# Kernel tuning notes

Measured on AMD Instinct MI355X. Metric: run time of the kernel, lower is better.

The kernel has to match this reference:

```python
import jax, jax.numpy as jnp
import numpy as np
import itertools


def setup_inputs() -> dict:
    key = jax.random.key(0)
    k1, k2 = jax.random.split(key)
    # Learned 3D LUT: [3, D, D, D], values in [0,1] like an identity/learned color LUT
    lut = jax.random.uniform(k1, (3, 33, 33, 33), dtype=jnp.float32)
    # Input RGB image batch in [0,1): [B, 3, H, W]
    x = jax.random.uniform(k2, (4, 3, 1080, 1920), dtype=jnp.float32)
    return {"lut": lut, "x": x}


def reference(lut, x):
    # Faithful JAX version of the trilinear.forward CUDA kernel:
    # per-pixel 8-corner trilinear interpolation into a [3, D, D, D] LUT.
    dim = lut.shape[-1]
    binsize = 1.000001 / (dim - 1)

    r, g, b = x[:, 0], x[:, 1], x[:, 2]  # each [B, H, W]

    inv = 1.0 / binsize
    rid = jnp.floor(r * inv).astype(jnp.int32)
    gid = jnp.floor(g * inv).astype(jnp.int32)
    bid = jnp.floor(b * inv).astype(jnp.int32)
    # fractional offsets within the cell
    fr = r * inv - rid
    fg = g * inv - gid
    fb = b * inv - bid
    # clamp so id+1 stays in range (kernel assumes x in [0,1))
    rid = jnp.clip(rid, 0, dim - 2)
    gid = jnp.clip(gid, 0, dim - 2)
    bid = jnp.clip(bid, 0, dim - 2)

    # LUT layout matches flattened index id_r + id_g*dim + id_b*dim^2
    # i.e. lut[c, b_idx, g_idx, r_idx].
    out = jnp.zeros((3,) + r.shape, dtype=x.dtype)  # [3, B, H, W]
    for db, dg, dr in itertools.product((0, 1), repeat=3):
        wr = fr if dr else (1.0 - fr)
        wg = fg if dg else (1.0 - fg)
        wb = fb if db else (1.0 - fb)
        w = wr * wg * wb  # [B, H, W]
        corner = lut[:, bid + db, gid + dg, rid + dr]  # [3, B, H, W] gather
        out = out + w[None] * corner

    return jnp.transpose(out, (1, 0, 2, 3))  # [B, 3, H, W]
```

## Files before the change

kernel.cpp:

```cpp
#include <hip/hip_runtime.h>
#include <hip/hip_fp16.h>

#define P_PLANE (1080*1920)
#define LUT_C   35937
#define N_IMG   4
#define SMEM_WORDS 35937
#define SMEM_BYTES (SMEM_WORDS * 4)

typedef float fvec4 __attribute__((ext_vector_type(4)));

__global__ __launch_bounds__(256) void build_lin_u8(const float* __restrict__ lut,
                                                    unsigned int* __restrict__ T) {
    int i = blockIdx.x * blockDim.x + threadIdx.x;
    if (i >= LUT_C) return;
    unsigned int r = (unsigned int)__float2int_rn(lut[i] * 255.0f);
    unsigned int g = (unsigned int)__float2int_rn(lut[LUT_C + i] * 255.0f);
    unsigned int b = (unsigned int)__float2int_rn(lut[2 * LUT_C + i] * 255.0f);
    T[i] = r | (g << 8) | (b << 16);
}

__device__ __forceinline__ float ub0(unsigned int e) { return (float)(e & 255u); }
__device__ __forceinline__ float ub1(unsigned int e) { return (float)((e >> 8) & 255u); }
__device__ __forceinline__ float ub2(unsigned int e) { return (float)((e >> 16) & 255u); }

__global__ __launch_bounds__(1024) void apply_lut_lds(const float* __restrict__ x,
                                                      const unsigned int* __restrict__ T,
                                                      float* __restrict__ out) {
    extern __shared__ unsigned int s_lut[];
    const int tid = threadIdx.x;

    {
        const uint4* Tv = (const uint4*)T;
        uint4* sv = (uint4*)s_lut;
        for (int i = tid; i < SMEM_WORDS / 4; i += blockDim.x) sv[i] = Tv[i];
        if (tid == 0) s_lut[SMEM_WORDS - 1] = T[SMEM_WORDS - 1];
    }
    __syncthreads();

    const float inv = (float)(1.0 / (1.000001 / 32.0));
    const float qs = 1.0f / 255.0f;
    const int QPI = P_PLANE / 4;
    const int total = N_IMG * QPI;

    for (int q = blockIdx.x * blockDim.x + tid; q < total; q += gridDim.x * blockDim.x) {
        int n  = q / QPI;
        int p4 = q - n * QPI;
        size_t base = (size_t)n * 3 * P_PLANE + (size_t)p4 * 4;

        fvec4 r4 = *(const fvec4*)(x + base);
        fvec4 g4 = *(const fvec4*)(x + base + P_PLANE);
        fvec4 b4 = *(const fvec4*)(x + base + 2 * P_PLANE);

        fvec4 vR, vG, vB;

#pragma unroll
        for (int i = 0; i < 4; ++i) {
            float tr = r4[i] * inv;
            float tg = g4[i] * inv;
            float tb = b4[i] * inv;
            float fr_ = floorf(tr), fg_ = floorf(tg), fb_ = floorf(tb);
            float fr = tr - fr_, fg = tg - fg_, fb = tb - fb_;
            int ri = min(max((int)fr_, 0), 31);
            int gi = min(max((int)fg_, 0), 31);
            int bi = min(max((int)fb_, 0), 31);
            int idx = bi * 1089 + gi * 33 + ri;

            unsigned int e000 = s_lut[idx],        e001 = s_lut[idx + 1];
            unsigned int e010 = s_lut[idx + 33],   e011 = s_lut[idx + 34];
            unsigned int e100 = s_lut[idx + 1089], e101 = s_lut[idx + 1090];
            unsigned int e110 = s_lut[idx + 1122], e111 = s_lut[idx + 1123];

            float wr1 = fr, wr0 = 1.0f - fr;
            float wg1 = fg, wg0 = 1.0f - fg;
            float wb1 = fb * qs, wb0 = (1.0f - fb) * qs;
            float w00 = wb0 * wg0, w01 = wb0 * wg1, w10 = wb1 * wg0, w11 = wb1 * wg1;
            float w000 = w00 * wr0, w001 = w00 * wr1;
            float w010 = w01 * wr0, w011 = w01 * wr1;
            float w100 = w10 * wr0, w101 = w10 * wr1;
            float w110 = w11 * wr0, w111 = w11 * wr1;

            float aR, aG, aB;
            aR = w000 * ub0(e000);            aG = w000 * ub1(e000);            aB = w000 * ub2(e000);
            aR = fmaf(w001, ub0(e001), aR);   aG = fmaf(w001, ub1(e001), aG);   aB = fmaf(w001, ub2(e001), aB);
            aR = fmaf(w010, ub0(e010), aR);   aG = fmaf(w010, ub1(e010), aG);   aB = fmaf(w010, ub2(e010), aB);
            aR = fmaf(w011, ub0(e011), aR);   aG = fmaf(w011, ub1(e011), aG);   aB = fmaf(w011, ub2(e011), aB);
            aR = fmaf(w100, ub0(e100), aR);   aG = fmaf(w100, ub1(e100), aG);   aB = fmaf(w100, ub2(e100), aB);
            aR = fmaf(w101, ub0(e101), aR);   aG = fmaf(w101, ub1(e101), aG);   aB = fmaf(w101, ub2(e101), aB);
            aR = fmaf(w110, ub0(e110), aR);   aG = fmaf(w110, ub1(e110), aG);   aB = fmaf(w110, ub2(e110), aB);
            aR = fmaf(w111, ub0(e111), aR);   aG = fmaf(w111, ub1(e111), aG);   aB = fmaf(w111, ub2(e111), aB);

            vR[i] = aR; vG[i] = aG; vB[i] = aB;
        }

        __builtin_nontemporal_store(vR, (fvec4*)(out + base));
        __builtin_nontemporal_store(vG, (fvec4*)(out + base + P_PLANE));
        __builtin_nontemporal_store(vB, (fvec4*)(out + base + 2 * P_PLANE));
    }
}

__global__ __launch_bounds__(256) void build_table(const float* __restrict__ lut,
                                                   uint4* __restrict__ T) {
    int cell = blockIdx.x * blockDim.x + threadIdx.x;
    int rid = cell & 31;
    int gid = (cell >> 5) & 31;
    int bid = cell >> 10;
    const float* b0 = lut + bid * 1089 + gid * 33 + rid;
    uint4 q[4];
    __half* h = (__half*)q;
#pragma unroll
    for (int k = 0; k < 8; ++k) {
        int off = (k >> 2) * 1089 + ((k >> 1) & 1) * 33 + (k & 1);
        h[k * 4 + 0] = __float2half(b0[off]);
        h[k * 4 + 1] = __float2half(b0[LUT_C + off]);
        h[k * 4 + 2] = __float2half(b0[2 * LUT_C + off]);
        h[k * 4 + 3] = __float2half(0.0f);
    }
    uint4* dst = T + (size_t)cell * 4;
    dst[0] = q[0]; dst[1] = q[1]; dst[2] = q[2]; dst[3] = q[3];
}

__device__ __forceinline__ void acc_chunk(const uint4& q, float wA, float wB,
                                          float& aR, float& aG, float& aB) {
    const __half* h = (const __half*)&q;
    aR = fmaf(wA, __half2float(h[0]), fmaf(wB, __half2float(h[4]), aR));
    aG = fmaf(wA, __half2float(h[1]), fmaf(wB, __half2float(h[5]), aG));
    aB = fmaf(wA, __half2float(h[2]), fmaf(wB, __half2float(h[6]), aB));
}

__global__ __launch_bounds__(256) void apply_lut(const float* __restrict__ x,
                                                 const __half* __restrict__ T,
                                                 float* __restrict__ out) {
    const float inv = (float)(1.0 / (1.000001 / 32.0));
    int n  = blockIdx.y;
    int i4 = blockIdx.x * blockDim.x + threadIdx.x;
    size_t base = (size_t)n * 3 * P_PLANE + (size_t)i4 * 4;

    float4 r4 = *(const float4*)(x + base);
    float4 g4 = *(const float4*)(x + base + P_PLANE);
    float4 b4 = *(const float4*)(x + base + 2 * P_PLANE);

    float r[4] = {r4.x, r4.y, r4.z, r4.w};
    float g[4] = {g4.x, g4.y, g4.z, g4.w};
    float b[4] = {b4.x, b4.y, b4.z, b4.w};
    float oR[4], oG[4], oB[4];

#pragma unroll
    for (int i = 0; i < 4; ++i) {
        float tr = r[i] * inv;
        float tg = g[i] * inv;
        float tb = b[i] * inv;
        float fr_ = floorf(tr), fg_ = floorf(tg), fb_ = floorf(tb);
        float fr = tr - fr_, fg = tg - fg_, fb = tb - fb_;
        int ri = min(max((int)fr_, 0), 31);
        int gi = min(max((int)fg_, 0), 31);
        int bi = min(max((int)fb_, 0), 31);

        const uint4* cp = (const uint4*)(T + ((size_t)(((bi << 5) | gi) << 5 | ri) << 5));
        uint4 q0 = cp[0], q1 = cp[1], q2 = cp[2], q3 = cp[3];

        float wr1 = fr, wr0 = 1.0f - fr;
        float wg1 = fg, wg0 = 1.0f - fg;
        float wb1 = fb, wb0 = 1.0f - fb;
        float w00 = wb0 * wg0, w01 = wb0 * wg1, w10 = wb1 * wg0, w11 = wb1 * wg1;

        float aR = 0.f, aG = 0.f, aB = 0.f;
        acc_chunk(q0, w00 * wr0, w00 * wr1, aR, aG, aB);
        acc_chunk(q1, w01 * wr0, w01 * wr1, aR, aG, aB);
        acc_chunk(q2, w10 * wr0, w10 * wr1, aR, aG, aB);
        acc_chunk(q3, w11 * wr0, w11 * wr1, aR, aG, aB);

        oR[i] = aR; oG[i] = aG; oB[i] = aB;
    }

    *(float4*)(out + base)               = make_float4(oR[0], oR[1], oR[2], oR[3]);
    *(float4*)(out + base + P_PLANE)     = make_float4(oG[0], oG[1], oG[2], oG[3]);
    *(float4*)(out + base + 2 * P_PLANE) = make_float4(oB[0], oB[1], oB[2], oB[3]);
}

extern "C" void kernel_launch(void* const* d_in, const int* in_sizes, int n_in,
                              void* d_out, int out_size, void* d_ws, size_t ws_size,
                              hipStream_t stream) {
    const float* lut = (const float*)d_in[0];
    const float* x   = (const float*)d_in[1];
    float* out = (float*)d_out;

    int dev = 0;
    (void)hipGetDevice(&dev);
    int max_shm = 0;
    (void)hipDeviceGetAttribute(&max_shm, hipDeviceAttributeMaxSharedMemoryPerBlock, dev);
    static_assert(SMEM_BYTES == 143748, "lut lds size");
    (void)hipFuncSetAttribute((const void*)apply_lut_lds,
                              hipFuncAttributeMaxDynamicSharedMemorySize, SMEM_BYTES);

    const size_t lin_bytes = (size_t)SMEM_BYTES;
    if (max_shm >= SMEM_BYTES && ws_size >= lin_bytes) {
        unsigned int* T = (unsigned int*)d_ws;
        build_lin_u8<<<(LUT_C + 255) / 256, 256, 0, stream>>>(lut, T);
        apply_lut_lds<<<256, 1024, SMEM_BYTES, stream>>>(x, T, out);
    } else {
        const size_t table_bytes = (size_t)32768 * 64;
        __half* T = (__half*)d_ws;
        build_table<<<128, 256, 0, stream>>>(lut, (uint4*)T);
        apply_lut<<<dim3(P_PLANE / (4 * 256), N_IMG), 256, 0, stream>>>(x, T, out);
    }
}
```

Baseline: 187.3 us.

## Software-pipeline input loads and process eight pixels per thread in LDS LUT kernel

The grid-stride loop is restructured so each thread handles eight pixels per iteration and prefetches the next iteration's input vectors before the current iteration's LDS gathers and FMAs run. All 64 LDS reads are issued before any arithmetic, which gives more memory-level parallelism. The host-side attribute queries are cached in a static variable, and launch_bounds gains a minimum-blocks hint. The cost is much higher register pressure, which could cause spills or reduce occupancy.

```diff
diff --git a/kernel.cpp b/kernel.cpp
--- a/kernel.cpp
+++ b/kernel.cpp
@@ -6,6 +6,9 @@
 #define N_IMG   4
 #define SMEM_WORDS 35937
 #define SMEM_BYTES (SMEM_WORDS * 4)
+
+#define PPI         (P_PLANE / 8)
+#define TOTAL_PAIRS (N_IMG * PPI)
 
 typedef float fvec4 __attribute__((ext_vector_type(4)));
 
@@ -23,9 +26,9 @@
 __device__ __forceinline__ float ub1(unsigned int e) { return (float)((e >> 8) & 255u); }
 __device__ __forceinline__ float ub2(unsigned int e) { return (float)((e >> 16) & 255u); }
 
-__global__ __launch_bounds__(1024) void apply_lut_lds(const float* __restrict__ x,
-                                                      const unsigned int* __restrict__ T,
-                                                      float* __restrict__ out) {
+__global__ __launch_bounds__(1024, 4) void apply_lut_lds(const float* __restrict__ x,
+                                                         const unsigned int* __restrict__ T,
+                                                         float* __restrict__ out) {
     extern __shared__ unsigned int s_lut[];
     const int tid = threadIdx.x;
 
@@ -39,62 +42,102 @@
 
     const float inv = (float)(1.0 / (1.000001 / 32.0));
     const float qs = 1.0f / 255.0f;
-    const int QPI = P_PLANE / 4;
-    const int total = N_IMG * QPI;
-
-    for (int q = blockIdx.x * blockDim.x + tid; q < total; q += gridDim.x * blockDim.x) {
-        int n  = q / QPI;
-        int p4 = q - n * QPI;
-        size_t base = (size_t)n * 3 * P_PLANE + (size_t)p4 * 4;
-
-        fvec4 r4 = *(const fvec4*)(x + base);
-        fvec4 g4 = *(const fvec4*)(x + base + P_PLANE);
-        fvec4 b4 = *(const fvec4*)(x + base + 2 * P_PLANE);
-
-        fvec4 vR, vG, vB;
-
-#pragma unroll
-        for (int i = 0; i < 4; ++i) {
-            float tr = r4[i] * inv;
-            float tg = g4[i] * inv;
-            float tb = b4[i] * inv;
+    const int stride = gridDim.x * blockDim.x;
+
+    int p = blockIdx.x * blockDim.x + tid;
+    if (p >= TOTAL_PAIRS) return;
+
+    size_t base;
+    {
+        int n = p / PPI;
+        base = (size_t)n * (3 * P_PLANE) + (size_t)(p - n * PPI) * 8;
+    }
+    fvec4 rA = *(const fvec4*)(x + base);
+    fvec4 rB = *(const fvec4*)(x + base + 4);
+    fvec4 gA = *(const fvec4*)(x + base + P_PLANE);
+    fvec4 gB = *(const fvec4*)(x + base + P_PLANE + 4);
+    fvec4 bA = *(const fvec4*)(x + base + 2 * P_PLANE);
+    fvec4 bB = *(const fvec4*)(x + base + 2 * P_PLANE + 4);
+
+    while (true) {
+        int pn = p + stride;
+        int pc = (pn < TOTAL_PAIRS) ? pn : p;
+        size_t nbase;
+        {
+            int n = pc / PPI;
+            nbase = (size_t)n * (3 * P_PLANE) + (size_t)(pc - n * PPI) * 8;
+        }
+        fvec4 nrA = *(const fvec4*)(x + nbase);
+        fvec4 nrB = *(const fvec4*)(x + nbase + 4);
+        fvec4 ngA = *(const fvec4*)(x + nbase + P_PLANE);
+        fvec4 ngB = *(const fvec4*)(x + nbase + P_PLANE + 4);
+        fvec4 nbA = *(const fvec4*)(x + nbase + 2 * P_PLANE);
+        fvec4 nbB = *(const fvec4*)(x + nbase + 2 * P_PLANE + 4);
+
+        int   idx[8];
+        float fr[8], fg[8], fb[8];
+#pragma unroll
+        for (int j = 0; j < 8; ++j) {
+            float r = (j < 4) ? rA[j] : rB[j - 4];
+            float g = (j < 4) ? gA[j] : gB[j - 4];
+            float b = (j < 4) ? bA[j] : bB[j - 4];
+            float tr = r * inv, tg = g * inv, tb = b * inv;
             float fr_ = floorf(tr), fg_ = floorf(tg), fb_ = floorf(tb);
-            float fr = tr - fr_, fg = tg - fg_, fb = tb - fb_;
+            fr[j] = tr - fr_; fg[j] = tg - fg_; fb[j] = tb - fb_;
             int ri = min(max((int)fr_, 0), 31);
             int gi = min(max((int)fg_, 0), 31);
             int bi = min(max((int)fb_, 0), 31);
-            int idx = bi * 1089 + gi * 33 + ri;
-
-            unsigned int e000 = s_lut[idx],        e001 = s_lut[idx + 1];
-            unsigned int e010 = s_lut[idx + 33],   e011 = s_lut[idx + 34];
-            unsigned int e100 = s_lut[idx + 1089], e101 = s_lut[idx + 1090];
-            unsigned int e110 = s_lut[idx + 1122], e111 = s_lut[idx + 1123];
-
-            float wr1 = fr, wr0 = 1.0f - fr;
-            float wg1 = fg, wg0 = 1.0f - fg;
-            float wb1 = fb * qs, wb0 = (1.0f - fb) * qs;
+            idx[j] = bi * 1089 + gi * 33 + ri;
+        }
+
+        unsigned int e[8][8];
+#pragma unroll
+        for (int j = 0; j < 8; ++j) {
+            int i0 = idx[j];
+            int i1 = idx[j] + 1089;
+            e[j][0] = s_lut[i0];       e[j][1] = s_lut[i0 + 1];
+            e[j][2] = s_lut[i0 + 33];  e[j][3] = s_lut[i0 + 34];
+            e[j][4] = s_lut[i1];       e[j][5] = s_lut[i1 + 1];
+            e[j][6] = s_lut[i1 + 33];  e[j][7] = s_lut[i1 + 34];
+        }
+
+        fvec4 oRA, oRB, oGA, oGB, oBA, oBB;
+#pragma unroll
+        for (int j = 0; j < 8; ++j) {
+            float wr1 = fr[j], wr0 = 1.0f - fr[j];
+            float wg1 = fg[j], wg0 = 1.0f - fg[j];
+            float wb1 = fb[j] * qs, wb0 = (1.0f - fb[j]) * qs;
             float w00 = wb0 * wg0, w01 = wb0 * wg1, w10 = wb1 * wg0, w11 = wb1 * wg1;
             float w000 = w00 * wr0, w001 = w00 * wr1;
             float w010 = w01 * wr0, w011 = w01 * wr1;
             float w100 = w10 * wr0, w101 = w10 * wr1;
             float w110 = w11 * wr0, w111 = w11 * wr1;
 
-            float aR, aG, aB;
-            aR = w000 * ub0(e000);            aG = w000 * ub1(e000);            aB = w000 * ub2(e000);
-            aR = fmaf(w001, ub0(e001), aR);   aG = fmaf(w001, ub1(e001), aG);   aB = fmaf(w001, ub2(e001), aB);
-            aR = fmaf(w010, ub0(e010), aR);   aG = fmaf(w010, ub1(e010), aG);   aB = fmaf(w010, ub2(e010), aB);
-            aR = fmaf(w011, ub0(e011), aR);   aG = fmaf(w011, ub1(e011), aG);   aB = fmaf(w011, ub2(e011), aB);
-            aR = fmaf(w100, ub0(e100), aR);   aG = fmaf(w100, ub1(e100), aG);   aB = fmaf(w100, ub2(e100), aB);
-            aR = fmaf(w101, ub0(e101), aR);   aG = fmaf(w101, ub1(e101), aG);   aB = fmaf(w101, ub2(e101), aB);
-            aR = fmaf(w110, ub0(e110), aR);   aG = fmaf(w110, ub1(e110), aG);   aB = fmaf(w110, ub2(e110), aB);
-            aR = fmaf(w111, ub0(e111), aR);   aG = fmaf(w111, ub1(e111), aG);   aB = fmaf(w111, ub2(e111), aB);
-
-            vR[i] = aR; vG[i] = aG; vB[i] = aB;
-        }
-
-        __builtin_nontemporal_store(vR, (fvec4*)(out + base));
-        __builtin_nontemporal_store(vG, (fvec4*)(out + base + P_PLANE));
-        __builtin_nontemporal_store(vB, (fvec4*)(out + base + 2 * P_PLANE));
+            float aR = w000 * ub0(e[j][0]);
+            float aG = w000 * ub1(e[j][0]);
+            float aB = w000 * ub2(e[j][0]);
+            aR = fmaf(w001, ub0(e[j][1]), aR); aG = fmaf(w001, ub1(e[j][1]), aG); aB = fmaf(w001, ub2(e[j][1]), aB);
+            aR = fmaf(w010, ub0(e[j][2]), aR); aG = fmaf(w010, ub1(e[j][2]), aG); aB = fmaf(w010, ub2(e[j][2]), aB);
+            aR = fmaf(w011, ub0(e[j][3]), aR); aG = fmaf(w011, ub1(e[j][3]), aG); aB = fmaf(w011, ub2(e[j][3]), aB);
+            aR = fmaf(w100, ub0(e[j][4]), aR); aG = fmaf(w100, ub1(e[j][4]), aG); aB = fmaf(w100, ub2(e[j][4]), aB);
+            aR = fmaf(w101, ub0(e[j][5]), aR); aG = fmaf(w101, ub1(e[j][5]), aG); aB = fmaf(w101, ub2(e[j][5]), aB);
+            aR = fmaf(w110, ub0(e[j][6]), aR); aG = fmaf(w110, ub1(e[j][6]), aG); aB = fmaf(w110, ub2(e[j][6]), aB);
+            aR = fmaf(w111, ub0(e[j][7]), aR); aG = fmaf(w111, ub1(e[j][7]), aG); aB = fmaf(w111, ub2(e[j][7]), aB);
+
+            if (j < 4) { oRA[j] = aR;     oGA[j] = aG;     oBA[j] = aB; }
+            else       { oRB[j - 4] = aR; oGB[j - 4] = aG; oBB[j - 4] = aB; }
+        }
+
+        __builtin_nontemporal_store(oRA, (fvec4*)(out + base));
+        __builtin_nontemporal_store(oRB, (fvec4*)(out + base + 4));
+        __builtin_nontemporal_store(oGA, (fvec4*)(out + base + P_PLANE));
+        __builtin_nontemporal_store(oGB, (fvec4*)(out + base + P_PLANE + 4));
+        __builtin_nontemporal_store(oBA, (fvec4*)(out + base + 2 * P_PLANE));
+        __builtin_nontemporal_store(oBB, (fvec4*)(out + base + 2 * P_PLANE + 4));
+
+        if (pn >= TOTAL_PAIRS) break;
+        p = pn; base = nbase;
+        rA = nrA; rB = nrB; gA = ngA; gB = ngB; bA = nbA; bB = nbB;
     }
 }
 
@@ -184,13 +227,16 @@
     const float* x   = (const float*)d_in[1];
     float* out = (float*)d_out;
 
-    int dev = 0;
-    (void)hipGetDevice(&dev);
-    int max_shm = 0;
-    (void)hipDeviceGetAttribute(&max_shm, hipDeviceAttributeMaxSharedMemoryPerBlock, dev);
-    static_assert(SMEM_BYTES == 143748, "lut lds size");
-    (void)hipFuncSetAttribute((const void*)apply_lut_lds,
-                              hipFuncAttributeMaxDynamicSharedMemorySize, SMEM_BYTES);
+    static int max_shm = -1;
+    if (max_shm < 0) {
+        int dev = 0;
+        (void)hipGetDevice(&dev);
+        (void)hipDeviceGetAttribute(&max_shm, hipDeviceAttributeMaxSharedMemoryPerBlock, dev);
+        static_assert(SMEM_BYTES == 143748, "lut lds size");
+        (void)hipFuncSetAttribute((const void*)apply_lut_lds,
+                                  hipFuncAttributeMaxDynamicSharedMemorySize, SMEM_BYTES);
+        if (max_shm < 0) max_shm = 0;
+    }
 
     const size_t lin_bytes = (size_t)SMEM_BYTES;
     if (max_shm >= SMEM_BYTES && ws_size >= lin_bytes) {
@@ -198,7 +244,6 @@
         build_lin_u8<<<(LUT_C + 255) / 256, 256, 0, stream>>>(lut, T);
         apply_lut_lds<<<256, 1024, SMEM_BYTES, stream>>>(x, T, out);
     } else {
-        const size_t table_bytes = (size_t)32768 * 64;
         __half* T = (__half*)d_ws;
         build_table<<<128, 256, 0, stream>>>(lut, (uint4*)T);
         apply_lut<<<dim3(P_PLANE / (4 * 256), N_IMG), 256, 0, stream>>>(x, T, out);
```

Result: slower. 205.8 us (+9.9%).

## Replace LDS-staged LUT with per-cell packed u8 corner table in global memory

Applied to the files above, without the earlier changes.

Builds a per-cell table holding all 8 corners as packed u8 RGB (32 bytes per cell) and gathers it with two 16-byte global loads per pixel, instead of staging the whole LUT into 140KB of LDS per block and doing 8 scattered LDS reads. This removes the per-block LDS fill and the occupancy limit of one large block per CU, relying on the 1MB table staying cache-resident. It also caches the device-attribute queries in a static and drops the old half-precision fallback path, so if the workspace is too small and LDS is insufficient nothing is launched.

```diff
diff --git a/kernel.cpp b/kernel.cpp
--- a/kernel.cpp
+++ b/kernel.cpp
@@ -7,45 +7,47 @@
 #define SMEM_WORDS 35937
 #define SMEM_BYTES (SMEM_WORDS * 4)
 
+#define N_CELLS   32768
+#define CELL_BYTES 32
+#define TABLE_BYTES ((size_t)N_CELLS * CELL_BYTES)
+
 typedef float fvec4 __attribute__((ext_vector_type(4)));
-
-__global__ __launch_bounds__(256) void build_lin_u8(const float* __restrict__ lut,
-                                                    unsigned int* __restrict__ T) {
-    int i = blockIdx.x * blockDim.x + threadIdx.x;
-    if (i >= LUT_C) return;
-    unsigned int r = (unsigned int)__float2int_rn(lut[i] * 255.0f);
-    unsigned int g = (unsigned int)__float2int_rn(lut[LUT_C + i] * 255.0f);
-    unsigned int b = (unsigned int)__float2int_rn(lut[2 * LUT_C + i] * 255.0f);
-    T[i] = r | (g << 8) | (b << 16);
-}
 
 __device__ __forceinline__ float ub0(unsigned int e) { return (float)(e & 255u); }
 __device__ __forceinline__ float ub1(unsigned int e) { return (float)((e >> 8) & 255u); }
 __device__ __forceinline__ float ub2(unsigned int e) { return (float)((e >> 16) & 255u); }
 
-__global__ __launch_bounds__(1024) void apply_lut_lds(const float* __restrict__ x,
-                                                      const unsigned int* __restrict__ T,
-                                                      float* __restrict__ out) {
-    extern __shared__ unsigned int s_lut[];
-    const int tid = threadIdx.x;
-
-    {
-        const uint4* Tv = (const uint4*)T;
-        uint4* sv = (uint4*)s_lut;
-        for (int i = tid; i < SMEM_WORDS / 4; i += blockDim.x) sv[i] = Tv[i];
-        if (tid == 0) s_lut[SMEM_WORDS - 1] = T[SMEM_WORDS - 1];
-    }
-    __syncthreads();
-
+__global__ __launch_bounds__(256) void build_cell_u8(const float* __restrict__ lut,
+                                                     uint4* __restrict__ T) {
+    int c = blockIdx.x * blockDim.x + threadIdx.x;
+    if (c >= N_CELLS) return;
+    int ri = c & 31, gi = (c >> 5) & 31, bi = c >> 10;
+    int idx = bi * 1089 + gi * 33 + ri;
+    unsigned int w[8];
+#pragma unroll
+    for (int k = 0; k < 8; ++k) {
+        int off = idx + (k & 1) + ((k >> 1) & 1) * 33 + ((k >> 2) & 1) * 1089;
+        unsigned int r = (unsigned int)__float2int_rn(lut[off] * 255.0f);
+        unsigned int g = (unsigned int)__float2int_rn(lut[LUT_C + off] * 255.0f);
+        unsigned int b = (unsigned int)__float2int_rn(lut[2 * LUT_C + off] * 255.0f);
+        w[k] = r | (g << 8) | (b << 16);
+    }
+    T[(size_t)c * 2]     = make_uint4(w[0], w[1], w[2], w[3]);
+    T[(size_t)c * 2 + 1] = make_uint4(w[4], w[5], w[6], w[7]);
+}
+
+__global__ __launch_bounds__(256, 8) void apply_lut_cell(const float* __restrict__ x,
+                                                         const uint4* __restrict__ T,
+                                                         float* __restrict__ out) {
     const float inv = (float)(1.0 / (1.000001 / 32.0));
     const float qs = 1.0f / 255.0f;
     const int QPI = P_PLANE / 4;
     const int total = N_IMG * QPI;
-
-    for (int q = blockIdx.x * blockDim.x + tid; q < total; q += gridDim.x * blockDim.x) {
-        int n  = q / QPI;
-        int p4 = q - n * QPI;
-        size_t base = (size_t)n * 3 * P_PLANE + (size_t)p4 * 4;
+    const int stride = gridDim.x * blockDim.x;
+
+    for (int q = blockIdx.x * blockDim.x + threadIdx.x; q < total; q += stride) {
+        int n = q / QPI;
+        size_t base = (size_t)n * (3 * P_PLANE) + (size_t)(q - n * QPI) * 4;
 
         fvec4 r4 = *(const fvec4*)(x + base);
         fvec4 g4 = *(const fvec4*)(x + base + P_PLANE);
@@ -63,12 +65,11 @@
             int ri = min(max((int)fr_, 0), 31);
             int gi = min(max((int)fg_, 0), 31);
             int bi = min(max((int)fb_, 0), 31);
-            int idx = bi * 1089 + gi * 33 + ri;
-
-            unsigned int e000 = s_lut[idx],        e001 = s_lut[idx + 1];
-            unsigned int e010 = s_lut[idx + 33],   e011 = s_lut[idx + 34];
-            unsigned int e100 = s_lut[idx + 1089], e101 = s_lut[idx + 1090];
-            unsigned int e110 = s_lut[idx + 1122], e111 = s_lut[idx + 1123];
+            int c = (bi << 10) | (gi << 5) | ri;
+
+            const uint4* cp = T + (size_t)c * 2;
+            uint4 lo = cp[0];
+            uint4 hi = cp[1];
 
             float wr1 = fr, wr0 = 1.0f - fr;
             float wg1 = fg, wg0 = 1.0f - fg;
@@ -79,15 +80,16 @@
             float w100 = w10 * wr0, w101 = w10 * wr1;
             float w110 = w11 * wr0, w111 = w11 * wr1;
 
-            float aR, aG, aB;
-            aR = w000 * ub0(e000);            aG = w000 * ub1(e000);            aB = w000 * ub2(e000);
-            aR = fmaf(w001, ub0(e001), aR);   aG = fmaf(w001, ub1(e001), aG);   aB = fmaf(w001, ub2(e001), aB);
-            aR = fmaf(w010, ub0(e010), aR);   aG = fmaf(w010, ub1(e010), aG);   aB = fmaf(w010, ub2(e010), aB);
-            aR = fmaf(w011, ub0(e011), aR);   aG = fmaf(w011, ub1(e011), aG);   aB = fmaf(w011, ub2(e011), aB);
-            aR = fmaf(w100, ub0(e100), aR);   aG = fmaf(w100, ub1(e100), aG);   aB = fmaf(w100, ub2(e100), aB);
-            aR = fmaf(w101, ub0(e101), aR);   aG = fmaf(w101, ub1(e101), aG);   aB = fmaf(w101, ub2(e101), aB);
-            aR = fmaf(w110, ub0(e110), aR);   aG = fmaf(w110, ub1(e110), aG);   aB = fmaf(w110, ub2(e110), aB);
-            aR = fmaf(w111, ub0(e111), aR);   aG = fmaf(w111, ub1(e111), aG);   aB = fmaf(w111, ub2(e111), aB);
+            float aR = w000 * ub0(lo.x);
+            float aG = w000 * ub1(lo.x);
+            float aB = w000 * ub2(lo.x);
+            aR = fmaf(w001, ub0(lo.y), aR); aG = fmaf(w001, ub1(lo.y), aG); aB = fmaf(w001, ub2(lo.y), aB);
+            aR = fmaf(w010, ub0(lo.z), aR); aG = fmaf(w010, ub1(lo.z), aG); aB = fmaf(w010, ub2(lo.z), aB);
+            aR = fmaf(w011, ub0(lo.w), aR); aG = fmaf(w011, ub1(lo.w), aG); aB = fmaf(w011, ub2(lo.w), aB);
+            aR = fmaf(w100, ub0(hi.x), aR); aG = fmaf(w100, ub1(hi.x), aG); aB = fmaf(w100, ub2(hi.x), aB);
+            aR = fmaf(w101, ub0(hi.y), aR); aG = fmaf(w101, ub1(hi.y), aG); aB = fmaf(w101, ub2(hi.y), aB);
+            aR = fmaf(w110, ub0(hi.z), aR); aG = fmaf(w110, ub1(hi.z), aG); aB = fmaf(w110, ub2(hi.z), aB);
+            aR = fmaf(w111, ub0(hi.w), aR); aG = fmaf(w111, ub1(hi.w), aG); aB = fmaf(w111, ub2(hi.w), aB);
 
             vR[i] = aR; vG[i] = aG; vB[i] = aB;
         }
@@ -98,83 +100,83 @@
     }
 }
 
-__global__ __launch_bounds__(256) void build_table(const float* __restrict__ lut,
-                                                   uint4* __restrict__ T) {
-    int cell = blockIdx.x * blockDim.x + threadIdx.x;
-    int rid = cell & 31;
-    int gid = (cell >> 5) & 31;
-    int bid = cell >> 10;
-    const float* b0 = lut + bid * 1089 + gid * 33 + rid;
-    uint4 q[4];
-    __half* h = (__half*)q;
+__global__ __launch_bounds__(256) void build_lin_u8(const float* __restrict__ lut,
+                                                    unsigned int* __restrict__ T) {
+    int i = blockIdx.x * blockDim.x + threadIdx.x;
+    if (i >= LUT_C) return;
+    unsigned int r = (unsigned int)__float2int_rn(lut[i] * 255.0f);
+    unsigned int g = (unsigned int)__float2int_rn(lut[LUT_C + i] * 255.0f);
+    unsigned int b = (unsigned int)__float2int_rn(lut[2 * LUT_C + i] * 255.0f);
+    T[i] = r | (g << 8) | (b << 16);
+}
+
+__global__ __launch_bounds__(1024, 4) void apply_lut_lds(const float* __restrict__ x,
+                                                         const unsigned int* __restrict__ T,
+                                                         float* __restrict__ out) {
+    extern __shared__ unsigned int s_lut[];
+    const int tid = threadIdx.x;
+    {
+        const uint4* Tv = (const uint4*)T;
+        uint4* sv = (uint4*)s_lut;
+        for (int i = tid; i < SMEM_WORDS / 4; i += blockDim.x) sv[i] = Tv[i];
+        if (tid == 0) s_lut[SMEM_WORDS - 1] = T[SMEM_WORDS - 1];
+    }
+    __syncthreads();
+
+    const float inv = (float)(1.0 / (1.000001 / 32.0));
+    const float qs = 1.0f / 255.0f;
+    const int QPI = P_PLANE / 4;
+    const int total = N_IMG * QPI;
+
+    for (int q = blockIdx.x * blockDim.x + tid; q < total; q += gridDim.x * blockDim.x) {
+        int n = q / QPI;
+        size_t base = (size_t)n * (3 * P_PLANE) + (size_t)(q - n * QPI) * 4;
+
+        fvec4 r4 = *(const fvec4*)(x + base);
+        fvec4 g4 = *(const fvec4*)(x + base + P_PLANE);
+        fvec4 b4 = *(const fvec4*)(x + base + 2 * P_PLANE);
+        fvec4 vR, vG, vB;
+
 #pragma unroll
-    for (int k = 0; k < 8; ++k) {
-        int off = (k >> 2) * 1089 + ((k >> 1) & 1) * 33 + (k & 1);
-        h[k * 4 + 0] = __float2half(b0[off]);
-        h[k * 4 + 1] = __float2half(b0[LUT_C + off]);
-        h[k * 4 + 2] = __float2half(b0[2 * LUT_C + off]);
-        h[k * 4 + 3] = __float2half(0.0f);
-    }
-    uint4* dst = T + (size_t)cell * 4;
-    dst[0] = q[0]; dst[1] = q[1]; dst[2] = q[2]; dst[3] = q[3];
-}
-
-__device__ __forceinline__ void acc_chunk(const uint4& q, float wA, float wB,
-                                          float& aR, float& aG, float& aB) {
-    const __half* h = (const __half*)&q;
-    aR = fmaf(wA, __half2float(h[0]), fmaf(wB, __half2float(h[4]), aR));
-    aG = fmaf(wA, __half2float(h[1]), fmaf(wB, __half2float(h[5]), aG));
-    aB = fmaf(wA, __half2float(h[2]), fmaf(wB, __half2float(h[6]), aB));
-}
-
-__global__ __launch_bounds__(256) void apply_lut(const float* __restrict__ x,
-                                                 const __half* __restrict__ T,
-                                                 float* __restrict__ out) {
-    const float inv = (float)(1.0 / (1.000001 / 32.0));
-    int n  = blockIdx.y;
-    int i4 = blockIdx.x * blockDim.x + threadIdx.x;
-    size_t base = (size_t)n * 3 * P_PLANE + (size_t)i4 * 4;
-
-    float4 r4 = *(const float4*)(x + base);
-    float4 g4 = *(const float4*)(x + base + P_PLANE);
-    float4 b4 = *(const float4*)(x + base + 2 * P_PLANE);
-
-    float r[4] = {r4.x, r4.y, r4.z, r4.w};
-    float g[4] = {g4.x, g4.y, g4.z, g4.w};
-    float b[4] = {b4.x, b4.y, b4.z, b4.w};
-    float oR[4], oG[4], oB[4];
-
-#pragma unroll
-    for (int i = 0; i < 4; ++i) {
-        float tr = r[i] * inv;
-        float tg = g[i] * inv;
-        float tb = b[i] * inv;
-        float fr_ = floorf(tr), fg_ = floorf(tg), fb_ = floorf(tb);
-        float fr = tr - fr_, fg = tg - fg_, fb = tb - fb_;
-        int ri = min(max((int)fr_, 0), 31);
-        int gi = min(max((int)fg_, 0), 31);
-        int bi = min(max((int)fb_, 0), 31);
-
-        const uint4* cp = (const uint4*)(T + ((size_t)(((bi << 5) | gi) << 5 | ri) << 5));
-        uint4 q0 = cp[0], q1 = cp[1], q2 = cp[2], q3 = cp[3];
-
-        float wr1 = fr, wr0 = 1.0f - fr;
-        float wg1 = fg, wg0 = 1.0f - fg;
-        float wb1 = fb, wb0 = 1.0f - fb;
-        float w00 = wb0 * wg0, w01 = wb0 * wg1, w10 = wb1 * wg0, w11 = wb1 * wg1;
-
-        float aR = 0.f, aG = 0.f, aB = 0.f;
-        acc_chunk(q0, w00 * wr0, w00 * wr1, aR, aG, aB);
-        acc_chunk(q1, w01 * wr0, w01 * wr1, aR, aG, aB);
-        acc_chunk(q2, w10 * wr0, w10 * wr1, aR, aG, aB);
-        acc_chunk(q3, w11 * wr0, w11 * wr1, aR, aG, aB);
-
-        oR[i] = aR; oG[i] = aG; oB[i] = aB;
-    }
-
-    *(float4*)(out + base)               = make_float4(oR[0], oR[1], oR[2], oR[3]);
-    *(float4*)(out + base + P_PLANE)     = make_float4(oG[0], oG[1], oG[2], oG[3]);
-    *(float4*)(out + base + 2 * P_PLANE) = make_float4(oB[0], oB[1], oB[2], oB[3]);
+        for (int i = 0; i < 4; ++i) {
+            float tr = r4[i] * inv, tg = g4[i] * inv, tb = b4[i] * inv;
+            float fr_ = floorf(tr), fg_ = floorf(tg), fb_ = floorf(tb);
+            float fr = tr - fr_, fg = tg - fg_, fb = tb - fb_;
+            int ri = min(max((int)fr_, 0), 31);
+            int gi = min(max((int)fg_, 0), 31);
+            int bi = min(max((int)fb_, 0), 31);
+            int idx = bi * 1089 + gi * 33 + ri;
+
+            unsigned int e000 = s_lut[idx],        e001 = s_lut[idx + 1];
+            unsigned int e010 = s_lut[idx + 33],   e011 = s_lut[idx + 34];
+            unsigned int e100 = s_lut[idx + 1089], e101 = s_lut[idx + 1090];
+            unsigned int e110 = s_lut[idx + 1122], e111 = s_lut[idx + 1123];
+
+            float wr1 = fr, wr0 = 1.0f - fr;
+            float wg1 = fg, wg0 = 1.0f - fg;
+            float wb1 = fb * qs, wb0 = (1.0f - fb) * qs;
+            float w00 = wb0 * wg0, w01 = wb0 * wg1, w10 = wb1 * wg0, w11 = wb1 * wg1;
+            float w000 = w00 * wr0, w001 = w00 * wr1;
+            float w010 = w01 * wr0, w011 = w01 * wr1;
+            float w100 = w10 * wr0, w101 = w10 * wr1;
+            float w110 = w11 * wr0, w111 = w11 * wr1;
+
+            float aR = w000 * ub0(e000), aG = w000 * ub1(e000), aB = w000 * ub2(e000);
+            aR = fmaf(w001, ub0(e001), aR); aG = fmaf(w001, ub1(e001), aG); aB = fmaf(w001, ub2(e001), aB);
+            aR = fmaf(w010, ub0(e010), aR); aG = fmaf(w010, ub1(e010), aG); aB = fmaf(w010, ub2(e010), aB);
+            aR = fmaf(w011, ub0(e011), aR); aG = fmaf(w011, ub1(e011), aG); aB = fmaf(w011, ub2(e011), aB);
+            aR = fmaf(w100, ub0(e100), aR); aG = fmaf(w100, ub1(e100), aG); aB = fmaf(w100, ub2(e100), aB);
+            aR = fmaf(w101, ub0(e101), aR); aG = fmaf(w101, ub1(e101), aG); aB = fmaf(w101, ub2(e101), aB);
+            aR = fmaf(w110, ub0(e110), aR); aG = fmaf(w110, ub1(e110), aG); aB = fmaf(w110, ub2(e110), aB);
+            aR = fmaf(w111, ub0(e111), aR); aG = fmaf(w111, ub1(e111), aG); aB = fmaf(w111, ub2(e111), aB);
+
+            vR[i] = aR; vG[i] = aG; vB[i] = aB;
+        }
+
+        __builtin_nontemporal_store(vR, (fvec4*)(out + base));
+        __builtin_nontemporal_store(vG, (fvec4*)(out + base + P_PLANE));
+        __builtin_nontemporal_store(vB, (fvec4*)(out + base + 2 * P_PLANE));
+    }
 }
 
 extern "C" void kernel_launch(void* const* d_in, const int* in_sizes, int n_in,
@@ -184,23 +186,24 @@
     const float* x   = (const float*)d_in[1];
     float* out = (float*)d_out;
 
-    int dev = 0;
-    (void)hipGetDevice(&dev);
-    int max_shm = 0;
-    (void)hipDeviceGetAttribute(&max_shm, hipDeviceAttributeMaxSharedMemoryPerBlock, dev);
-    static_assert(SMEM_BYTES == 143748, "lut lds size");
-    (void)hipFuncSetAttribute((const void*)apply_lut_lds,
-                              hipFuncAttributeMaxDynamicSharedMemorySize, SMEM_BYTES);
-
-    const size_t lin_bytes = (size_t)SMEM_BYTES;
-    if (max_shm >= SMEM_BYTES && ws_size >= lin_bytes) {
+    static int max_shm = -1;
+    if (max_shm < 0) {
+        int dev = 0;
+        (void)hipGetDevice(&dev);
+        (void)hipDeviceGetAttribute(&max_shm, hipDeviceAttributeMaxSharedMemoryPerBlock, dev);
+        static_assert(SMEM_BYTES == 143748, "lut lds size");
+        (void)hipFuncSetAttribute((const void*)apply_lut_lds,
+                                  hipFuncAttributeMaxDynamicSharedMemorySize, SMEM_BYTES);
+        if (max_shm < 0) max_shm = 0;
+    }
+
+    if (ws_size >= TABLE_BYTES) {
+        uint4* T = (uint4*)d_ws;
+        build_cell_u8<<<N_CELLS / 256, 256, 0, stream>>>(lut, T);
+        apply_lut_cell<<<2048, 256, 0, stream>>>(x, T, out);
+    } else if (max_shm >= SMEM_BYTES && ws_size >= (size_t)SMEM_BYTES) {
         unsigned int* T = (unsigned int*)d_ws;
         build_lin_u8<<<(LUT_C + 255) / 256, 256, 0, stream>>>(lut, T);
         apply_lut_lds<<<256, 1024, SMEM_BYTES, stream>>>(x, T, out);
-    } else {
-        const size_t table_bytes = (size_t)32768 * 64;
-        __half* T = (__half*)d_ws;
-        build_table<<<128, 256, 0, stream>>>(lut, (uint4*)T);
-        apply_lut<<<dim3(P_PLANE / (4 * 256), N_IMG), 256, 0, stream>>>(x, T, out);
-    }
-}
+    }
+}
```

Measured after the change: 457.4 us. 2.44x slower.

## Software-pipeline global loads ahead of LDS gathers in LUT apply loop

Applied to the files above, without the earlier changes.

The grid-stride loop in the LDS-resident LUT kernel is restructured so the next iteration's RGB input vectors are loaded from global memory while the current iteration's 32 LDS gathers and FMAs run. The gathers for all four pixels are also batched before any weights are computed, which exposes more memory-level parallelism. Launch bounds gain an occupancy hint, and the host-side device queries are cached in statics to cut per-call overhead. The cost is higher register pressure from holding prefetched inputs plus 32 gathered entries and weights at once.

```diff
diff --git a/kernel.cpp b/kernel.cpp
--- a/kernel.cpp
+++ b/kernel.cpp
@@ -8,6 +8,10 @@
 #define SMEM_BYTES (SMEM_WORDS * 4)
 
 typedef float fvec4 __attribute__((ext_vector_type(4)));
+
+__device__ __forceinline__ float ub0(unsigned int e) { return (float)(e & 255u); }
+__device__ __forceinline__ float ub1(unsigned int e) { return (float)((e >> 8) & 255u); }
+__device__ __forceinline__ float ub2(unsigned int e) { return (float)((e >> 16) & 255u); }
 
 __global__ __launch_bounds__(256) void build_lin_u8(const float* __restrict__ lut,
                                                     unsigned int* __restrict__ T) {
@@ -19,13 +23,9 @@
     T[i] = r | (g << 8) | (b << 16);
 }
 
-__device__ __forceinline__ float ub0(unsigned int e) { return (float)(e & 255u); }
-__device__ __forceinline__ float ub1(unsigned int e) { return (float)((e >> 8) & 255u); }
-__device__ __forceinline__ float ub2(unsigned int e) { return (float)((e >> 16) & 255u); }
-
-__global__ __launch_bounds__(1024) void apply_lut_lds(const float* __restrict__ x,
-                                                      const unsigned int* __restrict__ T,
-                                                      float* __restrict__ out) {
+__global__ __launch_bounds__(1024, 4) void apply_lut_lds(const float* __restrict__ x,
+                                                         const unsigned int* __restrict__ T,
+                                                         float* __restrict__ out) {
     extern __shared__ unsigned int s_lut[];
     const int tid = threadIdx.x;
 
@@ -41,60 +41,92 @@
     const float qs = 1.0f / 255.0f;
     const int QPI = P_PLANE / 4;
     const int total = N_IMG * QPI;
-
-    for (int q = blockIdx.x * blockDim.x + tid; q < total; q += gridDim.x * blockDim.x) {
-        int n  = q / QPI;
-        int p4 = q - n * QPI;
-        size_t base = (size_t)n * 3 * P_PLANE + (size_t)p4 * 4;
-
-        fvec4 r4 = *(const fvec4*)(x + base);
-        fvec4 g4 = *(const fvec4*)(x + base + P_PLANE);
-        fvec4 b4 = *(const fvec4*)(x + base + 2 * P_PLANE);
-
-        fvec4 vR, vG, vB;
-
-#pragma unroll
-        for (int i = 0; i < 4; ++i) {
-            float tr = r4[i] * inv;
-            float tg = g4[i] * inv;
-            float tb = b4[i] * inv;
+    const int G = gridDim.x * blockDim.x;
+
+    int q = blockIdx.x * blockDim.x + tid;
+    if (q >= total) return;
+
+    size_t base;
+    {
+        int n = q / QPI;
+        base = (size_t)n * (3 * P_PLANE) + (size_t)(q - n * QPI) * 4;
+    }
+    fvec4 r4 = *(const fvec4*)(x + base);
+    fvec4 g4 = *(const fvec4*)(x + base + P_PLANE);
+    fvec4 b4 = *(const fvec4*)(x + base + 2 * P_PLANE);
+
+    while (true) {
+        int   idx[4];
+        float fr[4], fg[4], fb[4];
+#pragma unroll
+        for (int i = 0; i < 4; ++i) {
+            float tr = r4[i] * inv, tg = g4[i] * inv, tb = b4[i] * inv;
             float fr_ = floorf(tr), fg_ = floorf(tg), fb_ = floorf(tb);
-            float fr = tr - fr_, fg = tg - fg_, fb = tb - fb_;
+            fr[i] = tr - fr_; fg[i] = tg - fg_; fb[i] = tb - fb_;
             int ri = min(max((int)fr_, 0), 31);
             int gi = min(max((int)fg_, 0), 31);
             int bi = min(max((int)fb_, 0), 31);
-            int idx = bi * 1089 + gi * 33 + ri;
-
-            unsigned int e000 = s_lut[idx],        e001 = s_lut[idx + 1];
-            unsigned int e010 = s_lut[idx + 33],   e011 = s_lut[idx + 34];
-            unsigned int e100 = s_lut[idx + 1089], e101 = s_lut[idx + 1090];
-            unsigned int e110 = s_lut[idx + 1122], e111 = s_lut[idx + 1123];
-
-            float wr1 = fr, wr0 = 1.0f - fr;
-            float wg1 = fg, wg0 = 1.0f - fg;
-            float wb1 = fb * qs, wb0 = (1.0f - fb) * qs;
+            idx[i] = bi * 1089 + gi * 33 + ri;
+        }
+
+        unsigned int e[4][8];
+#pragma unroll
+        for (int i = 0; i < 4; ++i) {
+            int i0 = idx[i];
+            int i1 = idx[i] + 1089;
+            e[i][0] = s_lut[i0];       e[i][1] = s_lut[i0 + 1];
+            e[i][2] = s_lut[i0 + 33];  e[i][3] = s_lut[i0 + 34];
+            e[i][4] = s_lut[i1];       e[i][5] = s_lut[i1 + 1];
+            e[i][6] = s_lut[i1 + 33];  e[i][7] = s_lut[i1 + 34];
+        }
+
+        int qn = q + G;
+        const bool more = (qn < total);
+        int qc = more ? qn : q;
+        size_t nbase;
+        {
+            int n = qc / QPI;
+            nbase = (size_t)n * (3 * P_PLANE) + (size_t)(qc - n * QPI) * 4;
+        }
+        fvec4 nr4 = *(const fvec4*)(x + nbase);
+        fvec4 ng4 = *(const fvec4*)(x + nbase + P_PLANE);
+        fvec4 nb4 = *(const fvec4*)(x + nbase + 2 * P_PLANE);
+
+        float w[4][8];
+#pragma unroll
+        for (int i = 0; i < 4; ++i) {
+            float wr1 = fr[i], wr0 = 1.0f - fr[i];
+            float wg1 = fg[i], wg0 = 1.0f - fg[i];
+            float wb1 = fb[i] * qs, wb0 = (1.0f - fb[i]) * qs;
             float w00 = wb0 * wg0, w01 = wb0 * wg1, w10 = wb1 * wg0, w11 = wb1 * wg1;
-            float w000 = w00 * wr0, w001 = w00 * wr1;
-            float w010 = w01 * wr0, w011 = w01 * wr1;
-            float w100 = w10 * wr0, w101 = w10 * wr1;
-            float w110 = w11 * wr0, w111 = w11 * wr1;
-
-            float aR, aG, aB;
-            aR = w000 * ub0(e000);            aG = w000 * ub1(e000);            aB = w000 * ub2(e000);
-            aR = fmaf(w001, ub0(e001), aR);   aG = fmaf(w001, ub1(e001), aG);   aB = fmaf(w001, ub2(e001), aB);
-            aR = fmaf(w010, ub0(e010), aR);   aG = fmaf(w010, ub1(e010), aG);   aB = fmaf(w010, ub2(e010), aB);
-            aR = fmaf(w011, ub0(e011), aR);   aG = fmaf(w011, ub1(e011), aG);   aB = fmaf(w011, ub2(e011), aB);
-            aR = fmaf(w100, ub0(e100), aR);   aG = fmaf(w100, ub1(e100), aG);   aB = fmaf(w100, ub2(e100), aB);
-            aR = fmaf(w101, ub0(e101), aR);   aG = fmaf(w101, ub1(e101), aG);   aB = fmaf(w101, ub2(e101), aB);
-            aR = fmaf(w110, ub0(e110), aR);   aG = fmaf(w110, ub1(e110), aG);   aB = fmaf(w110, ub2(e110), aB);
-            aR = fmaf(w111, ub0(e111), aR);   aG = fmaf(w111, ub1(e111), aG);   aB = fmaf(w111, ub2(e111), aB);
-
+            w[i][0] = w00 * wr0; w[i][1] = w00 * wr1;
+            w[i][2] = w01 * wr0; w[i][3] = w01 * wr1;
+            w[i][4] = w10 * wr0; w[i][5] = w10 * wr1;
+            w[i][6] = w11 * wr0; w[i][7] = w11 * wr1;
+        }
+
+        fvec4 vR, vG, vB;
+#pragma unroll
+        for (int i = 0; i < 4; ++i) {
+            float aR = w[i][0] * ub0(e[i][0]);
+            float aG = w[i][0] * ub1(e[i][0]);
+            float aB = w[i][0] * ub2(e[i][0]);
+#pragma unroll
+            for (int k = 1; k < 8; ++k) {
+                aR = fmaf(w[i][k], ub0(e[i][k]), aR);
+                aG = fmaf(w[i][k], ub1(e[i][k]), aG);
+                aB = fmaf(w[i][k], ub2(e[i][k]), aB);
+            }
             vR[i] = aR; vG[i] = aG; vB[i] = aB;
         }
 
         __builtin_nontemporal_store(vR, (fvec4*)(out + base));
         __builtin_nontemporal_store(vG, (fvec4*)(out + base + P_PLANE));
         __builtin_nontemporal_store(vB, (fvec4*)(out + base + 2 * P_PLANE));
+
+        if (!more) break;
+        q = qn; base = nbase;
+        r4 = nr4; g4 = ng4; b4 = nb4;
     }
 }
 
@@ -184,21 +216,22 @@
     const float* x   = (const float*)d_in[1];
     float* out = (float*)d_out;
 
-    int dev = 0;
-    (void)hipGetDevice(&dev);
-    int max_shm = 0;
-    (void)hipDeviceGetAttribute(&max_shm, hipDeviceAttributeMaxSharedMemoryPerBlock, dev);
-    static_assert(SMEM_BYTES == 143748, "lut lds size");
-    (void)hipFuncSetAttribute((const void*)apply_lut_lds,
-                              hipFuncAttributeMaxDynamicSharedMemorySize, SMEM_BYTES);
-
-    const size_t lin_bytes = (size_t)SMEM_BYTES;
-    if (max_shm >= SMEM_BYTES && ws_size >= lin_bytes) {
+    static int max_shm = -1;
+    if (max_shm < 0) {
+        int dev = 0;
+        (void)hipGetDevice(&dev);
+        (void)hipDeviceGetAttribute(&max_shm, hipDeviceAttributeMaxSharedMemoryPerBlock, dev);
+        static_assert(SMEM_BYTES == 143748, "lut lds size");
+        (void)hipFuncSetAttribute((const void*)apply_lut_lds,
+                                  hipFuncAttributeMaxDynamicSharedMemorySize, SMEM_BYTES);
+        if (max_shm < 0) max_shm = 0;
+    }
+
+    if (max_shm >= SMEM_BYTES && ws_size >= (size_t)SMEM_BYTES) {
         unsigned int* T = (unsigned int*)d_ws;
         build_lin_u8<<<(LUT_C + 255) / 256, 256, 0, stream>>>(lut, T);
         apply_lut_lds<<<256, 1024, SMEM_BYTES, stream>>>(x, T, out);
     } else {
-        const size_t table_bytes = (size_t)32768 * 64;
         __half* T = (__half*)d_ws;
         build_table<<<128, 256, 0, stream>>>(lut, (uint4*)T);
         apply_lut<<<dim3(P_PLANE / (4 * 256), N_IMG), 256, 0, stream>>>(x, T, out);
```

Result: no change. 187.6 us (+0.2%).
